# Performance work log

Hardware: AMD Instinct MI355X
Metric: run time of the kernel (lower is better)

Reference implementation:

```python
import jax, jax.numpy as jnp
import numpy as np

B, U, D_DEC, D_ENC = 32, 4096, 512, 512
ATT_UNITS, NUM_HEADS = 512, 4
HEAD_DIM = ATT_UNITS // NUM_HEADS
CONV_FILTERS, CONV_K = 32, 31
INIT = 0.075


def setup_inputs() -> dict:
    key = jax.random.key(0)
    ks = jax.random.split(key, 12)
    u = lambda k, shape: jax.random.uniform(k, shape, jnp.float32, -INIT, INIT)
    return {
        "dec_state": jax.random.normal(ks[0], (B, D_DEC), jnp.float32),
        "enc_state": jax.random.normal(ks[1], (B, U, D_ENC), jnp.float32),
        "prev_attention_weights": jax.random.uniform(ks[2], (B, U), jnp.float32),
        # stacked per-head Dense params
        "Wphi": u(ks[3], (NUM_HEADS, D_DEC, HEAD_DIM)),
        "bphi": jnp.zeros((NUM_HEADS, HEAD_DIM), jnp.float32),
        "Wpsi": u(ks[4], (NUM_HEADS, D_ENC, HEAD_DIM)),
        "bpsi": jnp.zeros((NUM_HEADS, HEAD_DIM), jnp.float32),
        # Conv1D kernel in WIO layout: (kernel_size, in_ch=1, out_ch=32), no bias
        "conv_kernel": jax.random.uniform(ks[5], (CONV_K, 1, CONV_FILTERS), jnp.float32, -0.1, 0.1),
        "Wloc": u(ks[6], (CONV_FILTERS, NUM_HEADS)),
        "Wout": u(ks[7], (NUM_HEADS * D_ENC, ATT_UNITS)),
        "bout": jnp.zeros((ATT_UNITS,), jnp.float32),
    }


def reference(dec_state, enc_state, prev_attention_weights,
              Wphi, bphi, Wpsi, bpsi, conv_kernel, Wloc, Wout, bout):
    # location features: Conv1D(same, no bias) over prev attention weights
    loc_feat = jax.lax.conv_general_dilated(
        prev_attention_weights[:, :, None], conv_kernel,
        window_strides=(1,), padding="SAME",
        dimension_numbers=("NWC", "WIO", "NWC"))            # (B, U, 32)
    loc_bias = loc_feat @ Wloc                                 # (B, U, H)
    loc_bias = jnp.transpose(loc_bias, (0, 2, 1))              # (B, H, U)

    # batched per-head projections (replaces the Python per-head loop)
    phi_s = jnp.einsum("bd,hdk->bhk", dec_state, Wphi) + bphi          # (B, H, hd)
    psi_h = jnp.einsum("bue,hek->bhuk", enc_state, Wpsi) + bpsi[:, None, :]  # (B, H, U, hd)

    energy = jnp.einsum("bhk,bhuk->bhu", phi_s, psi_h) + loc_bias      # (B, H, U)
    attn = jax.nn.softmax(energy, axis=-1)                              # (B, H, U)

    context = jnp.einsum("bhu,bue->bhe", attn, enc_state)               # (B, H, E)
    combined = context.reshape(context.shape[0], -1)                    # (B, H*E)
    context_vector = combined @ Wout + bout                             # (B, ATT_UNITS)
    attention_weights = jnp.mean(attn, axis=1)                          # (B, U)
    return context_vector, attention_weights
```

## Files before the change

kernel.cpp:

```cpp
#include <hip/hip_runtime.h>
#include <math.h>

#define B  32
#define U  4096
#define D  512
#define H  4
#define HD 128
#define CK 31
#define CF 32
#define AU 512

#define BPB    32
#define ROWS_W 32

static __device__ __forceinline__ float readlane_f(float v, int l) {
    return __int_as_float(__builtin_amdgcn_readlane(__float_as_int(v), l));
}

__global__ __launch_bounds__(256) void prep_kernel(
    const float* __restrict__ dec,
    const float* __restrict__ Wphi,
    const float* __restrict__ bphi,
    const float* __restrict__ Wpsi,
    const float* __restrict__ bpsi,
    const float* __restrict__ convk,
    const float* __restrict__ Wloc,
    float* __restrict__ ws_v,
    float* __restrict__ ws_const,
    float* __restrict__ ws_ck)
{
    __shared__ float decs[D];
    __shared__ float phis2[2][HD];
    __shared__ float phis[HD];
    const int b = blockIdx.x / H, h = blockIdx.x % H;
    const int tid = threadIdx.x;

    for (int i = tid; i < D; i += 256) decs[i] = dec[b * D + i];
    __syncthreads();

    {
        const int k = tid & 127, half = tid >> 7;
        const int d0 = half * 256;
        float acc = 0.f;
        const float* wp = Wphi + (size_t)h * D * HD + (size_t)d0 * HD + k;
        #pragma unroll 8
        for (int d = 0; d < 256; ++d) acc += decs[d0 + d] * wp[(size_t)d * HD];
        phis2[half][k] = acc;
    }
    __syncthreads();
    if (tid < HD) phis[tid] = phis2[0][tid] + phis2[1][tid] + bphi[h * HD + tid];
    __syncthreads();

    if (tid == 0) {
        float c = 0.f;
        for (int k = 0; k < HD; ++k) c += phis[k] * bpsi[h * HD + k];
        ws_const[b * H + h] = c;
    }

    for (int e = tid; e < D; e += 256) {
        const float* wq = Wpsi + ((size_t)h * D + e) * HD;
        float acc = 0.f;
        #pragma unroll 8
        for (int k = 0; k < HD; ++k) acc += wq[k] * phis[k];
        ws_v[((size_t)b * H + h) * D + e] = acc;
    }

    if (blockIdx.x == 0 && tid < CK * H) {
        int t = tid / H, hh = tid % H;
        float acc = 0.f;
        for (int f = 0; f < CF; ++f) acc += convk[t * CF + f] * Wloc[f * H + hh];
        ws_ck[t * H + hh] = acc;
    }
}

__global__ __launch_bounds__(256, 4) void fused_pass1(
    const float* __restrict__ enc,
    const float* __restrict__ prevw,
    const float* __restrict__ ws_v,
    const float* __restrict__ ws_const,
    const float* __restrict__ ws_ck,
    float* __restrict__ energy,
    float* __restrict__ pctx,
    float* __restrict__ pms)
{
    const int b    = blockIdx.y;
    const int blk  = blockIdx.x;
    const int tid  = threadIdx.x;
    const int lane = tid & 63;
    const int wave = tid >> 6;
    const int ubase = (blk * 4 + wave) * ROWS_W;

    __shared__ float lctx[4][H][D];
    __shared__ float lms[4][H][2];
    __shared__ float lalpha[H][4];

    float4 v0[H], v1[H];
    #pragma unroll
    for (int h = 0; h < H; ++h) {
        const float* vp = ws_v + ((size_t)b * H + h) * D + lane * 8;
        v0[h] = *(const float4*)vp;
        v1[h] = *(const float4*)(vp + 4);
    }
    float ckr[H] = {0.f, 0.f, 0.f, 0.f};
    if (lane < CK) {
        #pragma unroll
        for (int h = 0; h < H; ++h) ckr[h] = ws_ck[lane * H + h];
    }
    float ct[H];
    #pragma unroll
    for (int h = 0; h < H; ++h) ct[h] = ws_const[b * H + h];

    float w0;
    {
        const int gi = ubase - 15 + lane;
        w0 = (gi >= 0 && gi < U) ? prevw[b * U + gi] : 0.f;
    }

    float m0 = -3.402823466e38f, m1 = m0, m2 = m0, m3 = m0;
    float s0 = 0.f, s1 = 0.f, s2 = 0.f, s3 = 0.f;
    float4 z = {0.f, 0.f, 0.f, 0.f};
    float4 c00 = z, c01 = z, c10 = z, c11 = z, c20 = z, c21 = z, c30 = z, c31 = z;

    const bool b16 = (lane & 16) != 0;
    const bool b32 = (lane & 32) != 0;

    const float* encb = enc + ((size_t)b * U + ubase) * D + lane * 8;
    float4 e0 = *(const float4*)encb;
    float4 e1 = *(const float4*)(encb + 4);

    for (int r = 0; r < ROWS_W; ++r) {
        float4 n0, n1;
        if (r < ROWS_W - 1) {
            const float* nx = encb + (size_t)(r + 1) * D;
            n0 = *(const float4*)nx;
            n1 = *(const float4*)(nx + 4);
        }
        const int u = ubase + r;
        float pw = __int_as_float(
            __builtin_amdgcn_ds_bpermute((r + lane) << 2, __float_as_int(w0)));

        float p0 = pw * ckr[0]
            + e0.x*v0[0].x + e0.y*v0[0].y + e0.z*v0[0].z + e0.w*v0[0].w
            + e1.x*v1[0].x + e1.y*v1[0].y + e1.z*v1[0].z + e1.w*v1[0].w;
        float p1 = pw * ckr[1]
            + e0.x*v0[1].x + e0.y*v0[1].y + e0.z*v0[1].z + e0.w*v0[1].w
            + e1.x*v1[1].x + e1.y*v1[1].y + e1.z*v1[1].z + e1.w*v1[1].w;
        float p2 = pw * ckr[2]
            + e0.x*v0[2].x + e0.y*v0[2].y + e0.z*v0[2].z + e0.w*v0[2].w
            + e1.x*v1[2].x + e1.y*v1[2].y + e1.z*v1[2].z + e1.w*v1[2].w;
        float p3 = pw * ckr[3]
            + e0.x*v0[3].x + e0.y*v0[3].y + e0.z*v0[3].z + e0.w*v0[3].w
            + e1.x*v1[3].x + e1.y*v1[3].y + e1.z*v1[3].z + e1.w*v1[3].w;

        float keepA = b16 ? p1 : p0, sendA = b16 ? p0 : p1;
        float a  = keepA + __shfl_xor(sendA, 16);
        float keepB = b16 ? p3 : p2, sendB = b16 ? p2 : p3;
        float bb = keepB + __shfl_xor(sendB, 16);
        float keepC = b32 ? bb : a, sendC = b32 ? a : bb;
        float c = keepC + __shfl_xor(sendC, 32);
        c += __shfl_xor(c, 1);
        c += __shfl_xor(c, 2);
        c += __shfl_xor(c, 4);
        c += __shfl_xor(c, 8);
        float eh0 = readlane_f(c, 0)  + ct[0];
        float eh1 = readlane_f(c, 16) + ct[1];
        float eh2 = readlane_f(c, 32) + ct[2];
        float eh3 = readlane_f(c, 48) + ct[3];

        if (lane < H) {
            float ev = (lane == 0) ? eh0 : (lane == 1) ? eh1 : (lane == 2) ? eh2 : eh3;
            energy[((size_t)b * H + lane) * U + u] = ev;
        }

        float mn0 = fmaxf(m0, eh0), mn1 = fmaxf(m1, eh1);
        float mn2 = fmaxf(m2, eh2), mn3 = fmaxf(m3, eh3);
        if (mn0 > m0 || mn1 > m1 || mn2 > m2 || mn3 > m3) {
            float a0 = __expf(m0 - mn0), a1 = __expf(m1 - mn1);
            float a2 = __expf(m2 - mn2), a3 = __expf(m3 - mn3);
            s0 *= a0; s1 *= a1; s2 *= a2; s3 *= a3;
            c00.x*=a0; c00.y*=a0; c00.z*=a0; c00.w*=a0; c01.x*=a0; c01.y*=a0; c01.z*=a0; c01.w*=a0;
            c10.x*=a1; c10.y*=a1; c10.z*=a1; c10.w*=a1; c11.x*=a1; c11.y*=a1; c11.z*=a1; c11.w*=a1;
            c20.x*=a2; c20.y*=a2; c20.z*=a2; c20.w*=a2; c21.x*=a2; c21.y*=a2; c21.z*=a2; c21.w*=a2;
            c30.x*=a3; c30.y*=a3; c30.z*=a3; c30.w*=a3; c31.x*=a3; c31.y*=a3; c31.z*=a3; c31.w*=a3;
            m0 = mn0; m1 = mn1; m2 = mn2; m3 = mn3;
        }
        float w0e = __expf(eh0 - m0), w1e = __expf(eh1 - m1);
        float w2e = __expf(eh2 - m2), w3e = __expf(eh3 - m3);
        s0 += w0e; s1 += w1e; s2 += w2e; s3 += w3e;
        c00.x += w0e*e0.x; c00.y += w0e*e0.y; c00.z += w0e*e0.z; c00.w += w0e*e0.w;
        c01.x += w0e*e1.x; c01.y += w0e*e1.y; c01.z += w0e*e1.z; c01.w += w0e*e1.w;
        c10.x += w1e*e0.x; c10.y += w1e*e0.y; c10.z += w1e*e0.z; c10.w += w1e*e0.w;
        c11.x += w1e*e1.x; c11.y += w1e*e1.y; c11.z += w1e*e1.z; c11.w += w1e*e1.w;
        c20.x += w2e*e0.x; c20.y += w2e*e0.y; c20.z += w2e*e0.z; c20.w += w2e*e0.w;
        c21.x += w2e*e1.x; c21.y += w2e*e1.y; c21.z += w2e*e1.z; c21.w += w2e*e1.w;
        c30.x += w3e*e0.x; c30.y += w3e*e0.y; c30.z += w3e*e0.z; c30.w += w3e*e0.w;
        c31.x += w3e*e1.x; c31.y += w3e*e1.y; c31.z += w3e*e1.z; c31.w += w3e*e1.w;

        e0 = n0; e1 = n1;
    }

    *(float4*)&lctx[wave][0][lane * 8]     = c00;
    *(float4*)&lctx[wave][0][lane * 8 + 4] = c01;
    *(float4*)&lctx[wave][1][lane * 8]     = c10;
    *(float4*)&lctx[wave][1][lane * 8 + 4] = c11;
    *(float4*)&lctx[wave][2][lane * 8]     = c20;
    *(float4*)&lctx[wave][2][lane * 8 + 4] = c21;
    *(float4*)&lctx[wave][3][lane * 8]     = c30;
    *(float4*)&lctx[wave][3][lane * 8 + 4] = c31;
    if (lane == 0) {
        lms[wave][0][0] = m0; lms[wave][0][1] = s0;
        lms[wave][1][0] = m1; lms[wave][1][1] = s1;
        lms[wave][2][0] = m2; lms[wave][2][1] = s2;
        lms[wave][3][0] = m3; lms[wave][3][1] = s3;
    }
    __syncthreads();

    const size_t pbase = ((size_t)(b * BPB + blk)) * H;
    if (tid < H) {
        const int h = tid;
        float M = fmaxf(fmaxf(lms[0][h][0], lms[1][h][0]),
                        fmaxf(lms[2][h][0], lms[3][h][0]));
        float S = 0.f;
        #pragma unroll
        for (int w = 0; w < 4; ++w) {
            float al = __expf(lms[w][h][0] - M);
            lalpha[h][w] = al;
            S += al * lms[w][h][1];
        }
        pms[(pbase + h) * 2]     = M;
        pms[(pbase + h) * 2 + 1] = S;
    }
    __syncthreads();

    #pragma unroll
    for (int h = 0; h < H; ++h) {
        const float a0 = lalpha[h][0], a1 = lalpha[h][1];
        const float a2 = lalpha[h][2], a3 = lalpha[h][3];
        #pragma unroll
        for (int half = 0; half < 2; ++half) {
            const int d = tid + half * 256;
            float val = a0 * lctx[0][h][d] + a1 * lctx[1][h][d]
                      + a2 * lctx[2][h][d] + a3 * lctx[3][h][d];
            pctx[(pbase + h) * D + d] = val;
        }
    }
}

__global__ __launch_bounds__(256) void combine_kernel(
    const float* __restrict__ pctx,
    const float* __restrict__ pms,
    float* __restrict__ ctx,
    float* __restrict__ MS)
{
    const int bh = blockIdx.x;
    const int b = bh >> 2, h = bh & 3;
    const int tid = threadIdx.x;
    __shared__ float sm[BPB], ss[BPB], salpha[BPB];
    __shared__ float MSsh[2];

    if (tid < BPB) {
        sm[tid] = pms[(((size_t)b * BPB + tid) * H + h) * 2];
        ss[tid] = pms[(((size_t)b * BPB + tid) * H + h) * 2 + 1];
    }
    __syncthreads();
    if (tid == 0) {
        float M = -3.402823466e38f;
        for (int i = 0; i < BPB; ++i) M = fmaxf(M, sm[i]);
        float S = 0.f;
        for (int i = 0; i < BPB; ++i) {
            float al = __expf(sm[i] - M);
            salpha[i] = al;
            S += al * ss[i];
        }
        MSsh[0] = M; MSsh[1] = S;
        MS[bh * 2] = M; MS[bh * 2 + 1] = S;
    }
    __syncthreads();
    const float invS = 1.0f / MSsh[1];

    float acc0 = 0.f, acc1 = 0.f;
    const float* base = pctx + ((size_t)b * BPB * H + h) * D;
    #pragma unroll 4
    for (int i = 0; i < BPB; ++i) {
        float al = salpha[i];
        const float* p = base + (size_t)i * H * D;
        acc0 += al * p[tid];
        acc1 += al * p[tid + 256];
    }
    ctx[(size_t)bh * D + tid]       = acc0 * invS;
    ctx[(size_t)bh * D + tid + 256] = acc1 * invS;
}

__global__ __launch_bounds__(256) void attw_kernel(
    const float* __restrict__ energy,
    const float* __restrict__ MS,
    float* __restrict__ attw)
{
    const int b = blockIdx.x, tid = threadIdx.x;
    float M[H], iS[H];
    #pragma unroll
    for (int h = 0; h < H; ++h) {
        M[h]  = MS[(b * H + h) * 2];
        iS[h] = 1.0f / MS[(b * H + h) * 2 + 1];
    }
    #pragma unroll
    for (int i = 0; i < 16; ++i) {
        const int u = tid + i * 256;
        float acc = 0.f;
        #pragma unroll
        for (int h = 0; h < H; ++h)
            acc += __expf(energy[((size_t)b * H + h) * U + u] - M[h]) * iS[h];
        attw[(size_t)b * U + u] = acc * 0.25f;
    }
}

__global__ __launch_bounds__(256) void outproj_kernel(
    const float* __restrict__ ctx,
    const float* __restrict__ Wout,
    const float* __restrict__ bout,
    float* __restrict__ outv)
{
    const int b = blockIdx.y;
    const int j = blockIdx.x * 256 + threadIdx.x;
    const int i0 = blockIdx.z * 256;
    __shared__ float c_s[256];
    c_s[threadIdx.x] = ctx[(size_t)b * (H * D) + i0 + threadIdx.x];
    __syncthreads();

    float acc = (blockIdx.z == 0) ? bout[j] : 0.f;
    #pragma unroll 8
    for (int i = 0; i < 256; ++i)
        acc += c_s[i] * Wout[(size_t)(i0 + i) * AU + j];
    atomicAdd(&outv[(size_t)b * AU + j], acc);
}

extern "C" void kernel_launch(void* const* d_in, const int* in_sizes, int n_in,
                              void* d_out, int out_size, void* d_ws, size_t ws_size,
                              hipStream_t stream) {
    const float* dec   = (const float*)d_in[0];
    const float* enc   = (const float*)d_in[1];
    const float* prevw = (const float*)d_in[2];
    const float* Wphi  = (const float*)d_in[3];
    const float* bphi  = (const float*)d_in[4];
    const float* Wpsi  = (const float*)d_in[5];
    const float* bpsi  = (const float*)d_in[6];
    const float* convk = (const float*)d_in[7];
    const float* Wloc  = (const float*)d_in[8];
    const float* Wout  = (const float*)d_in[9];
    const float* bout  = (const float*)d_in[10];

    float* out  = (float*)d_out;
    float* outv = out;
    float* attw = out + B * AU;

    float* ws        = (float*)d_ws;
    float* ws_v      = ws;
    float* ws_const  = ws + 65536;
    float* ws_ck     = ws + 65664;
    float* ws_energy = ws + 65792;
    float* ws_pctx   = ws_energy + (size_t)B*H*U;
    float* ws_pms    = ws_pctx + (size_t)B*BPB*H*D;
    float* ws_MS     = ws_pms + (size_t)B*BPB*H*2;
    float* ws_ctx    = ws_MS + 256;

    hipMemsetAsync(outv, 0, (size_t)B * AU * sizeof(float), stream);

    prep_kernel<<<dim3(B * H), 256, 0, stream>>>(dec, Wphi, bphi, Wpsi, bpsi,
                                                 convk, Wloc, ws_v, ws_const, ws_ck);
    fused_pass1<<<dim3(BPB, B), 256, 0, stream>>>(enc, prevw, ws_v, ws_const,
                                                  ws_ck, ws_energy, ws_pctx, ws_pms);
    combine_kernel<<<dim3(B * H), 256, 0, stream>>>(ws_pctx, ws_pms, ws_ctx, ws_MS);
    attw_kernel<<<dim3(B), 256, 0, stream>>>(ws_energy, ws_MS, attw);
    outproj_kernel<<<dim3(2, B, 8), 256, 0, stream>>>(ws_ctx, Wout, bout, outv);
}
```

Measured before the change: 437.8 us.

## Use exp2 with prescaled logits, fuse combine with out-projection, widen attw grid

The per-head vectors and constants are prescaled by log2(e) so every softmax exponential becomes a native exp2 instruction. Each lane's encoder loads are rearranged into two coalesced float4 halves of the row instead of 8 contiguous floats. The combine and output-projection kernels are merged so the context stays in shared memory and one launch disappears. The attention-weight kernel is spread over many more blocks. The trade-off is that the fused out-projection runs on only 128 blocks, each reading a full 512x512 Wout slice, so it has less parallelism than the previous 512-block projection.

```diff
diff --git a/kernel.cpp b/kernel.cpp
--- a/kernel.cpp
+++ b/kernel.cpp
@@ -13,8 +13,13 @@
 #define BPB    32
 #define ROWS_W 32
 
+#define LOG2E 1.4426950408889634f
+
 static __device__ __forceinline__ float readlane_f(float v, int l) {
     return __int_as_float(__builtin_amdgcn_readlane(__float_as_int(v), l));
+}
+static __device__ __forceinline__ float fast_exp2(float x) {
+    return __builtin_amdgcn_exp2f(x);
 }
 
 __global__ __launch_bounds__(256) void prep_kernel(
@@ -54,7 +59,7 @@
     if (tid == 0) {
         float c = 0.f;
         for (int k = 0; k < HD; ++k) c += phis[k] * bpsi[h * HD + k];
-        ws_const[b * H + h] = c;
+        ws_const[b * H + h] = c * LOG2E;
     }
 
     for (int e = tid; e < D; e += 256) {
@@ -62,14 +67,14 @@
         float acc = 0.f;
         #pragma unroll 8
         for (int k = 0; k < HD; ++k) acc += wq[k] * phis[k];
-        ws_v[((size_t)b * H + h) * D + e] = acc;
+        ws_v[((size_t)b * H + h) * D + e] = acc * LOG2E;
     }
 
     if (blockIdx.x == 0 && tid < CK * H) {
         int t = tid / H, hh = tid % H;
         float acc = 0.f;
         for (int f = 0; f < CF; ++f) acc += convk[t * CF + f] * Wloc[f * H + hh];
-        ws_ck[t * H + hh] = acc;
+        ws_ck[t * H + hh] = acc * LOG2E;
     }
 }
 
@@ -97,9 +102,9 @@
     float4 v0[H], v1[H];
     #pragma unroll
     for (int h = 0; h < H; ++h) {
-        const float* vp = ws_v + ((size_t)b * H + h) * D + lane * 8;
-        v0[h] = *(const float4*)vp;
-        v1[h] = *(const float4*)(vp + 4);
+        const float* vp = ws_v + ((size_t)b * H + h) * D;
+        v0[h] = *(const float4*)(vp + lane * 4);
+        v1[h] = *(const float4*)(vp + 256 + lane * 4);
     }
     float ckr[H] = {0.f, 0.f, 0.f, 0.f};
     if (lane < CK) {
@@ -124,16 +129,16 @@
     const bool b16 = (lane & 16) != 0;
     const bool b32 = (lane & 32) != 0;
 
-    const float* encb = enc + ((size_t)b * U + ubase) * D + lane * 8;
-    float4 e0 = *(const float4*)encb;
-    float4 e1 = *(const float4*)(encb + 4);
+    const float* encb = enc + ((size_t)b * U + ubase) * D;
+    float4 e0 = *(const float4*)(encb + lane * 4);
+    float4 e1 = *(const float4*)(encb + 256 + lane * 4);
 
     for (int r = 0; r < ROWS_W; ++r) {
         float4 n0, n1;
         if (r < ROWS_W - 1) {
             const float* nx = encb + (size_t)(r + 1) * D;
-            n0 = *(const float4*)nx;
-            n1 = *(const float4*)(nx + 4);
+            n0 = *(const float4*)(nx + lane * 4);
+            n1 = *(const float4*)(nx + 256 + lane * 4);
         }
         const int u = ubase + r;
         float pw = __int_as_float(
@@ -175,8 +180,8 @@
         float mn0 = fmaxf(m0, eh0), mn1 = fmaxf(m1, eh1);
         float mn2 = fmaxf(m2, eh2), mn3 = fmaxf(m3, eh3);
         if (mn0 > m0 || mn1 > m1 || mn2 > m2 || mn3 > m3) {
-            float a0 = __expf(m0 - mn0), a1 = __expf(m1 - mn1);
-            float a2 = __expf(m2 - mn2), a3 = __expf(m3 - mn3);
+            float a0 = fast_exp2(m0 - mn0), a1 = fast_exp2(m1 - mn1);
+            float a2 = fast_exp2(m2 - mn2), a3 = fast_exp2(m3 - mn3);
             s0 *= a0; s1 *= a1; s2 *= a2; s3 *= a3;
             c00.x*=a0; c00.y*=a0; c00.z*=a0; c00.w*=a0; c01.x*=a0; c01.y*=a0; c01.z*=a0; c01.w*=a0;
             c10.x*=a1; c10.y*=a1; c10.z*=a1; c10.w*=a1; c11.x*=a1; c11.y*=a1; c11.z*=a1; c11.w*=a1;
@@ -184,8 +189,8 @@
             c30.x*=a3; c30.y*=a3; c30.z*=a3; c30.w*=a3; c31.x*=a3; c31.y*=a3; c31.z*=a3; c31.w*=a3;
             m0 = mn0; m1 = mn1; m2 = mn2; m3 = mn3;
         }
-        float w0e = __expf(eh0 - m0), w1e = __expf(eh1 - m1);
-        float w2e = __expf(eh2 - m2), w3e = __expf(eh3 - m3);
+        float w0e = fast_exp2(eh0 - m0), w1e = fast_exp2(eh1 - m1);
+        float w2e = fast_exp2(eh2 - m2), w3e = fast_exp2(eh3 - m3);
         s0 += w0e; s1 += w1e; s2 += w2e; s3 += w3e;
         c00.x += w0e*e0.x; c00.y += w0e*e0.y; c00.z += w0e*e0.z; c00.w += w0e*e0.w;
         c01.x += w0e*e1.x; c01.y += w0e*e1.y; c01.z += w0e*e1.z; c01.w += w0e*e1.w;
@@ -199,14 +204,14 @@
         e0 = n0; e1 = n1;
     }
 
-    *(float4*)&lctx[wave][0][lane * 8]     = c00;
-    *(float4*)&lctx[wave][0][lane * 8 + 4] = c01;
-    *(float4*)&lctx[wave][1][lane * 8]     = c10;
-    *(float4*)&lctx[wave][1][lane * 8 + 4] = c11;
-    *(float4*)&lctx[wave][2][lane * 8]     = c20;
-    *(float4*)&lctx[wave][2][lane * 8 + 4] = c21;
-    *(float4*)&lctx[wave][3][lane * 8]     = c30;
-    *(float4*)&lctx[wave][3][lane * 8 + 4] = c31;
+    *(float4*)&lctx[wave][0][lane * 4]       = c00;
+    *(float4*)&lctx[wave][0][256 + lane * 4] = c01;
+    *(float4*)&lctx[wave][1][lane * 4]       = c10;
+    *(float4*)&lctx[wave][1][256 + lane * 4] = c11;
+    *(float4*)&lctx[wave][2][lane * 4]       = c20;
+    *(float4*)&lctx[wave][2][256 + lane * 4] = c21;
+    *(float4*)&lctx[wave][3][lane * 4]       = c30;
+    *(float4*)&lctx[wave][3][256 + lane * 4] = c31;
     if (lane == 0) {
         lms[wave][0][0] = m0; lms[wave][0][1] = s0;
         lms[wave][1][0] = m1; lms[wave][1][1] = s1;
@@ -223,7 +228,7 @@
         float S = 0.f;
         #pragma unroll
         for (int w = 0; w < 4; ++w) {
-            float al = __expf(lms[w][h][0] - M);
+            float al = fast_exp2(lms[w][h][0] - M);
             lalpha[h][w] = al;
             S += al * lms[w][h][1];
         }
@@ -246,10 +251,12 @@
     }
 }
 
-__global__ __launch_bounds__(256) void combine_kernel(
+__global__ __launch_bounds__(256) void combine_outproj_kernel(
     const float* __restrict__ pctx,
     const float* __restrict__ pms,
-    float* __restrict__ ctx,
+    const float* __restrict__ Wout,
+    const float* __restrict__ bout,
+    float* __restrict__ outv,
     float* __restrict__ MS)
 {
     const int bh = blockIdx.x;
@@ -257,6 +264,7 @@
     const int tid = threadIdx.x;
     __shared__ float sm[BPB], ss[BPB], salpha[BPB];
     __shared__ float MSsh[2];
+    __shared__ float c_s[D];
 
     if (tid < BPB) {
         sm[tid] = pms[(((size_t)b * BPB + tid) * H + h) * 2];
@@ -268,7 +276,7 @@
         for (int i = 0; i < BPB; ++i) M = fmaxf(M, sm[i]);
         float S = 0.f;
         for (int i = 0; i < BPB; ++i) {
-            float al = __expf(sm[i] - M);
+            float al = fast_exp2(sm[i] - M);
             salpha[i] = al;
             S += al * ss[i];
         }
@@ -287,8 +295,21 @@
         acc0 += al * p[tid];
         acc1 += al * p[tid + 256];
     }
-    ctx[(size_t)bh * D + tid]       = acc0 * invS;
-    ctx[(size_t)bh * D + tid + 256] = acc1 * invS;
+    c_s[tid]       = acc0 * invS;
+    c_s[tid + 256] = acc1 * invS;
+    __syncthreads();
+
+    float a0 = (h == 0) ? bout[tid]       : 0.f;
+    float a1 = (h == 0) ? bout[tid + 256] : 0.f;
+    const float* W = Wout + (size_t)h * D * AU;
+    #pragma unroll 8
+    for (int i = 0; i < D; ++i) {
+        const float ci = c_s[i];
+        a0 += ci * W[(size_t)i * AU + tid];
+        a1 += ci * W[(size_t)i * AU + tid + 256];
+    }
+    atomicAdd(&outv[(size_t)b * AU + tid],       a0);
+    atomicAdd(&outv[(size_t)b * AU + tid + 256], a1);
 }
 
 __global__ __launch_bounds__(256) void attw_kernel(
@@ -296,42 +317,16 @@
     const float* __restrict__ MS,
     float* __restrict__ attw)
 {
-    const int b = blockIdx.x, tid = threadIdx.x;
-    float M[H], iS[H];
+    const int b = blockIdx.x;
+    const int u = blockIdx.y * 256 + threadIdx.x;
+    float acc = 0.f;
     #pragma unroll
     for (int h = 0; h < H; ++h) {
-        M[h]  = MS[(b * H + h) * 2];
-        iS[h] = 1.0f / MS[(b * H + h) * 2 + 1];
-    }
-    #pragma unroll
-    for (int i = 0; i < 16; ++i) {
-        const int u = tid + i * 256;
-        float acc = 0.f;
-        #pragma unroll
-        for (int h = 0; h < H; ++h)
-            acc += __expf(energy[((size_t)b * H + h) * U + u] - M[h]) * iS[h];
-        attw[(size_t)b * U + u] = acc * 0.25f;
-    }
-}
-
-__global__ __launch_bounds__(256) void outproj_kernel(
-    const float* __restrict__ ctx,
-    const float* __restrict__ Wout,
-    const float* __restrict__ bout,
-    float* __restrict__ outv)
-{
-    const int b = blockIdx.y;
-    const int j = blockIdx.x * 256 + threadIdx.x;
-    const int i0 = blockIdx.z * 256;
-    __shared__ float c_s[256];
-    c_s[threadIdx.x] = ctx[(size_t)b * (H * D) + i0 + threadIdx.x];
-    __syncthreads();
-
-    float acc = (blockIdx.z == 0) ? bout[j] : 0.f;
-    #pragma unroll 8
-    for (int i = 0; i < 256; ++i)
-        acc += c_s[i] * Wout[(size_t)(i0 + i) * AU + j];
-    atomicAdd(&outv[(size_t)b * AU + j], acc);
+        const float M  = MS[(b * H + h) * 2];
+        const float iS = 1.0f / MS[(b * H + h) * 2 + 1];
+        acc += fast_exp2(energy[((size_t)b * H + h) * U + u] - M) * iS;
+    }
+    attw[(size_t)b * U + u] = acc * 0.25f;
 }
 
 extern "C" void kernel_launch(void* const* d_in, const int* in_sizes, int n_in,
@@ -361,7 +356,6 @@
     float* ws_pctx   = ws_energy + (size_t)B*H*U;
     float* ws_pms    = ws_pctx + (size_t)B*BPB*H*D;
     float* ws_MS     = ws_pms + (size_t)B*BPB*H*2;
-    float* ws_ctx    = ws_MS + 256;
 
     hipMemsetAsync(outv, 0, (size_t)B * AU * sizeof(float), stream);
 
@@ -369,7 +363,7 @@
                                                  convk, Wloc, ws_v, ws_const, ws_ck);
     fused_pass1<<<dim3(BPB, B), 256, 0, stream>>>(enc, prevw, ws_v, ws_const,
                                                   ws_ck, ws_energy, ws_pctx, ws_pms);
-    combine_kernel<<<dim3(B * H), 256, 0, stream>>>(ws_pctx, ws_pms, ws_ctx, ws_MS);
-    attw_kernel<<<dim3(B), 256, 0, stream>>>(ws_energy, ws_MS, attw);
-    outproj_kernel<<<dim3(2, B, 8), 256, 0, stream>>>(ws_ctx, Wout, bout, outv);
-}
+    combine_outproj_kernel<<<dim3(B * H), 256, 0, stream>>>(ws_pctx, ws_pms, Wout,
+                                                            bout, outv, ws_MS);
+    attw_kernel<<<dim3(B, U / 256), 256, 0, stream>>>(ws_energy, ws_MS, attw);
+}
```

Result: slower. 451.9 us (+3.2%).
